# Performance work log

Measured on AMD Instinct MI355X. Metric: run time of the kernel, lower is better.

## Reference

```python
import jax, jax.numpy as jnp
import numpy as np

EPS = 1e-05
K = 32


def _knn_idx(xyz_B3N, k):
    # negative squared pairwise distance: -||xi||^2 + 2 xi.xj - ||xj||^2
    inner = 2.0 * jnp.einsum('bdn,bdm->bnm', xyz_B3N, xyz_B3N)  # [B,N,N]
    xx = jnp.sum(xyz_B3N ** 2, axis=1)  # [B,N]
    pd = inner - xx[:, :, None] - xx[:, None, :]
    _, idx = jax.lax.top_k(pd, k)  # [B,N,k] nearest (largest negative dist)
    return idx


def setup_inputs() -> dict:
    key = jax.random.key(0)
    k1, k2 = jax.random.split(key)
    B, N, C = 16, 4096, 64
    xyz_B3N = jax.random.normal(k1, (B, 3, N), dtype=jnp.float32)
    feats_BNC = jax.random.normal(k2, (B, N, C), dtype=jnp.float32)
    alpha = jnp.ones((C,), dtype=jnp.float32)
    beta = jnp.zeros((C,), dtype=jnp.float32)
    return {"xyz_B3N": xyz_B3N, "feats_BNC": feats_BNC, "alpha": alpha, "beta": beta}


def reference(xyz_B3N, feats_BNC, alpha, beta):
    idx = _knn_idx(xyz_B3N, K)  # [B,N,k]
    # gather neighbor features directly: [B,N,k,C]
    neigh = jax.vmap(lambda f, i: f[i])(feats_BNC, idx)
    offset = neigh - feats_BNC[:, :, None, :]  # [B,N,k,C]
    sigma = jnp.mean(offset ** 2)  # global scalar
    gaed = (offset / (sigma + EPS)) * alpha + beta
    pooled = jnp.max(gaed, axis=2)  # [B,N,C]
    return pooled
```

## Files before the change

kernel.cpp:

```cpp
#include <hip/hip_runtime.h>
#include <float.h>

#define BB 16
#define NN 4096
#define CC 64
#define KNN 32
#define NSLICE 16
#define SSZ 256
#define CKEEP 8
#define NQ 65536


__device__ __forceinline__ int lane_rank(unsigned long long m) {
    return __builtin_amdgcn_mbcnt_hi((unsigned)(m >> 32),
           __builtin_amdgcn_mbcnt_lo((unsigned)m, 0u));
}

__device__ __forceinline__ unsigned med3u(unsigned a, unsigned b, unsigned c) {
    unsigned d;
    asm("v_med3_u32 %0, %1, %2, %3" : "=v"(d) : "v"(a), "v"(b), "v"(c));
    return d;
}

#define UCHAIN8 \
  h07=med3u(ky,h07,h06); h06=med3u(ky,h06,h05); h05=med3u(ky,h05,h04); \
  h04=med3u(ky,h04,h03); h03=med3u(ky,h03,h02); h02=med3u(ky,h02,h01); \
  h01=med3u(ky,h01,h00); h00=(h00>ky)?h00:ky;

__global__ __launch_bounds__(256) void prep_kernel(
        const float* __restrict__ xyz, float4* __restrict__ pts4,
        int* __restrict__ flag_cnt) {
#pragma clang fp contract(off)
    const int p = blockIdx.x * 256 + threadIdx.x;
    if (p == 0) flag_cnt[0] = 0;
    const int b = p >> 12;
    const int i = p & (NN - 1);
    const float* xb = xyz + (size_t)b * (3 * NN);
    float x = xb[i], y = xb[NN + i], z = xb[2 * NN + i];
    float xx = ((x * x) + (y * y)) + (z * z);
    pts4[p] = make_float4(x, y, z, xx);
}

__global__ __launch_bounds__(256) void knn_select_kernel(
        const float4* __restrict__ pts4, unsigned* __restrict__ val_buf) {
#pragma clang fp contract(off)
    __shared__ float4 pts[SSZ];
    const int tid = threadIdx.x;
    const int blk = blockIdx.x;
    const int s = blk & 15;
    const int g = (blk >> 4) & 15;
    const int b = blk >> 8;
    const float4* pb = pts4 + (b << 12);

    pts[tid] = pb[(s << 8) | tid];
    const int q = (g << 8) | tid;
    const float4 qp = pb[q];
    const float qx = qp.x, qy = qp.y, qz = qp.z;
    const float nqxx = -qp.w;
    __syncthreads();

    unsigned h00=0,h01=0,h02=0,h03=0,h04=0,h05=0,h06=0,h07=0;
    const unsigned ibase = 4095u - (unsigned)(s << 8);
#pragma unroll 4
    for (int j = 0; j < SSZ; ++j) {
        float4 cp = pts[j];
        float dot = __builtin_fmaf(qz, cp.z, __builtin_fmaf(qy, cp.y, qx * cp.x));
        float pd = __builtin_fmaf(2.0f, dot, nqxx) - cp.w;
        pd = fminf(pd, 0.0f);
        unsigned ky = (~__float_as_uint(pd) & 0xFFFFF000u)
                      | (ibase - (unsigned)j);
        UCHAIN8
    }

    const int qg = (b << 12) | q;
    unsigned* vp = val_buf + (size_t)(s * CKEEP) * NQ + qg;
#define ST(t, ht) vp[(size_t)(t) * NQ] = ht;
    ST(0,h00) ST(1,h01) ST(2,h02) ST(3,h03)
    ST(4,h04) ST(5,h05) ST(6,h06) ST(7,h07)
#undef ST
}

__global__ __launch_bounds__(64) void knn_merge_kernel(
        const unsigned* __restrict__ val_buf, int* __restrict__ idx_out,
        int* __restrict__ flag_list, int* __restrict__ flag_cnt) {
    __shared__ unsigned lv[64 * 129];
    const int tid = threadIdx.x;
    const int qg = blockIdx.x * 64 + tid;
    unsigned* my = lv + tid * 129;
    for (int t = 0; t < 128; ++t) my[t] = val_buf[(size_t)t * NQ + qg];

    int p0=0,p1=0,p2=0,p3=0,p4=0,p5=0,p6=0,p7=0,
        p8=0,p9=0,p10=0,p11=0,p12=0,p13=0,p14=0,p15=0;
    unsigned v0 =my[0],  v1 =my[8],  v2 =my[16],  v3 =my[24];
    unsigned v4 =my[32], v5 =my[40], v6 =my[48],  v7 =my[56];
    unsigned v8 =my[64], v9 =my[72], v10=my[80],  v11=my[88];
    unsigned v12=my[96], v13=my[104],v14=my[112], v15=my[120];
    int* outp = idx_out + (size_t)qg * KNN;
    unsigned key32 = 0u, key33 = 0u;
    for (int step = 0; step < 33; ++step) {
        unsigned best = v0; int bp = 0;
        if (v1  > best) { best = v1;  bp = 1; }
        if (v2  > best) { best = v2;  bp = 2; }
        if (v3  > best) { best = v3;  bp = 3; }
        if (v4  > best) { best = v4;  bp = 4; }
        if (v5  > best) { best = v5;  bp = 5; }
        if (v6  > best) { best = v6;  bp = 6; }
        if (v7  > best) { best = v7;  bp = 7; }
        if (v8  > best) { best = v8;  bp = 8; }
        if (v9  > best) { best = v9;  bp = 9; }
        if (v10 > best) { best = v10; bp = 10; }
        if (v11 > best) { best = v11; bp = 11; }
        if (v12 > best) { best = v12; bp = 12; }
        if (v13 > best) { best = v13; bp = 13; }
        if (v14 > best) { best = v14; bp = 14; }
        if (v15 > best) { best = v15; bp = 15; }
        if (step == 32) { key33 = best; break; }
        outp[step] = 4095 - (int)(best & 4095u);
        if (step == 31) key32 = best;
        if      (bp==0)  { ++p0;  v0  = (p0 <8)?my[p0]      :0u; }
        else if (bp==1)  { ++p1;  v1  = (p1 <8)?my[8+p1]    :0u; }
        else if (bp==2)  { ++p2;  v2  = (p2 <8)?my[16+p2]   :0u; }
        else if (bp==3)  { ++p3;  v3  = (p3 <8)?my[24+p3]   :0u; }
        else if (bp==4)  { ++p4;  v4  = (p4 <8)?my[32+p4]   :0u; }
        else if (bp==5)  { ++p5;  v5  = (p5 <8)?my[40+p5]   :0u; }
        else if (bp==6)  { ++p6;  v6  = (p6 <8)?my[48+p6]   :0u; }
        else if (bp==7)  { ++p7;  v7  = (p7 <8)?my[56+p7]   :0u; }
        else if (bp==8)  { ++p8;  v8  = (p8 <8)?my[64+p8]   :0u; }
        else if (bp==9)  { ++p9;  v9  = (p9 <8)?my[72+p9]   :0u; }
        else if (bp==10) { ++p10; v10 = (p10<8)?my[80+p10]  :0u; }
        else if (bp==11) { ++p11; v11 = (p11<8)?my[88+p11]  :0u; }
        else if (bp==12) { ++p12; v12 = (p12<8)?my[96+p12]  :0u; }
        else if (bp==13) { ++p13; v13 = (p13<8)?my[104+p13] :0u; }
        else if (bp==14) { ++p14; v14 = (p14<8)?my[112+p14] :0u; }
        else             { ++p15; v15 = (p15<8)?my[120+p15] :0u; }
    }

    bool flag = ((key32 >> 12) == (key33 >> 12));
    for (int sl = 0; sl < 16; ++sl)
        flag = flag || (my[sl * 8 + 7] >= key33);
    if (flag) {
        int pos = atomicAdd(flag_cnt, 1);
        flag_list[pos] = qg;
    }
}

__global__ __launch_bounds__(256) void knn_fallback_kernel(
        const float* __restrict__ xyz, const int* __restrict__ flag_list,
        const int* __restrict__ flag_cnt, int* __restrict__ idx_out) {
#pragma clang fp contract(off)
    const int nflag = flag_cnt[0];
    const int lane = threadIdx.x & 63;
    const int wid = (blockIdx.x * 256 + threadIdx.x) >> 6;
    const int nw = (gridDim.x * 256) >> 6;
    for (int w = wid; w < nflag; w += nw) {
        const int qg = flag_list[w];
        const int b = qg >> 12;
        const int q = qg & (NN - 1);
        const float* xb = xyz + (size_t)b * (3 * NN);
        const float qx = xb[q], qy = xb[NN + q], qz = xb[2 * NN + q];
        const float qxx = ((qx * qx) + (qy * qy)) + (qz * qz);
        const float nqxx = -qxx;

        unsigned key[64];
#pragma unroll
        for (int i = 0; i < 64; ++i) {
            const int j = (i << 6) | lane;
            float x = xb[j], y = xb[NN + j], z = xb[2 * NN + j];
            float xxc = ((x * x) + (y * y)) + (z * z);
            float dot = __builtin_fmaf(qz, z, __builtin_fmaf(qy, y, qx * x));
            float pd = __builtin_fmaf(2.0f, dot, nqxx) - xxc;
            unsigned u = __float_as_uint(pd);
            key[i] = u ^ (unsigned)(((int)u >> 31) | 0x80000000);
        }

        unsigned cur = 0u;
        for (int bit = 31; bit >= 0; --bit) {
            const unsigned cand = cur | (1u << bit);
            int c = 0;
#pragma unroll
            for (int i = 0; i < 64; ++i) c += (key[i] >= cand) ? 1 : 0;
#pragma unroll
            for (int o = 32; o >= 1; o >>= 1) c += __shfl_xor(c, o, 64);
            if (c >= 32) cur = cand;
        }

        int ge = 0;
#pragma unroll
        for (int i = 0; i < 64; ++i) {
            ge += (key[i] > cur) ? 1 : 0;
            ge += (key[i] == cur) ? 0x10000 : 0;
        }
#pragma unroll
        for (int o = 32; o >= 1; o >>= 1) ge += __shfl_xor(ge, o, 64);
        const int gt_total = ge & 0xFFFF;
        const int budget = min(ge >> 16, 32 - gt_total);

        int* outp = idx_out + (size_t)qg * KNN;
        int slot = 0, neq = 0;
#pragma unroll
        for (int i = 0; i < 64; ++i) {
            const bool isgt = key[i] > cur;
            const bool iseq = key[i] == cur;
            const unsigned long long mgt = __ballot(isgt);
            const unsigned long long meq = __ballot(iseq);
            if (isgt) outp[slot + lane_rank(mgt)] = (i << 6) | lane;
            if (iseq) {
                const int r = neq + lane_rank(meq);
                if (r < budget) outp[gt_total + r] = (i << 6) | lane;
            }
            slot += __builtin_popcountll(mgt);
            neq += __builtin_popcountll(meq);
        }
    }
}

__global__ __launch_bounds__(256) void gather_minmax_kernel(
        const float* __restrict__ feats, const int* __restrict__ idx_in,
        float* __restrict__ mx_buf, float* __restrict__ mn_buf,
        double* __restrict__ partials) {
    const int tid = threadIdx.x;
    const int w = tid >> 6;
    const int lane = tid & 63;
    const int q = blockIdx.x * 4 + w;
    const int b = q >> 12;
    const float* fb = feats + (size_t)b * (NN * CC);
    const float center = feats[(size_t)q * CC + lane];
    const int* ip = idx_in + (size_t)q * KNN;

    float mx = -FLT_MAX, mn = FLT_MAX;
    double ss = 0.0;
#pragma unroll 4
    for (int k = 0; k < KNN; ++k) {
        int nb = ip[k];
        float v = fb[(size_t)nb * CC + lane];
        float off = v - center;
        mx = fmaxf(mx, off);
        mn = fminf(mn, off);
        double od = (double)off;
        ss = fma(od, od, ss);
    }
    mx_buf[(size_t)q * CC + lane] = mx;
    mn_buf[(size_t)q * CC + lane] = mn;

#pragma unroll
    for (int o = 32; o >= 1; o >>= 1) ss += __shfl_down(ss, o, 64);
    __shared__ double wsum[4];
    if (lane == 0) wsum[w] = ss;
    __syncthreads();
    if (tid == 0) partials[blockIdx.x] = (wsum[0] + wsum[1]) + (wsum[2] + wsum[3]);
}

__global__ __launch_bounds__(1024) void sigma_kernel(const double* __restrict__ partials,
                                                     float* __restrict__ sigma) {
    __shared__ double red[1024];
    double s = 0.0;
    for (int i = threadIdx.x; i < 16384; i += 1024) s += partials[i];
    red[threadIdx.x] = s;
    __syncthreads();
    for (int o = 512; o >= 1; o >>= 1) {
        if (threadIdx.x < o) red[threadIdx.x] += red[threadIdx.x + o];
        __syncthreads();
    }
    if (threadIdx.x == 0) sigma[0] = (float)(red[0] * (1.0 / 134217728.0));
}

__global__ __launch_bounds__(256) void finalize_kernel(
        const float* __restrict__ mx_buf, const float* __restrict__ mn_buf,
        const float* __restrict__ alpha, const float* __restrict__ beta,
        const float* __restrict__ sigma, float* __restrict__ out) {
#pragma clang fp contract(off)
    const int e = blockIdx.x * 256 + threadIdx.x;
    const int c = e & (CC - 1);
    const float s = sigma[0] + 1e-5f;
    const float a = alpha[c];
    const float bt = beta[c];
    const float off = (a >= 0.f) ? mx_buf[e] : mn_buf[e];
    const float t = off / s;
    out[e] = (t * a) + bt;
}

extern "C" void kernel_launch(void* const* d_in, const int* in_sizes, int n_in,
                              void* d_out, int out_size, void* d_ws, size_t ws_size,
                              hipStream_t stream) {
    (void)in_sizes; (void)n_in; (void)out_size; (void)ws_size;
    const float* xyz   = (const float*)d_in[0];
    const float* feats = (const float*)d_in[1];
    const float* alpha = (const float*)d_in[2];
    const float* beta  = (const float*)d_in[3];
    float* out = (float*)d_out;

    char* ws = (char*)d_ws;
    unsigned* val_buf  = (unsigned*)ws;
    float*    mx_buf   = (float*)ws;
    float*    mn_buf   = (float*)(ws + 16777216);
    int*      idx_buf  = (int*)(ws + 33554432);
    int*      flag_list= (int*)(ws + 41943040);
    int*      flag_cnt = (int*)(ws + 42205184);
    float4*   pts4     = (float4*)(ws + 42205248);
    double*   partials = (double*)(ws + 42205248);
    float*    sigma    = (float*)(ws + 43254784);

    prep_kernel<<<NQ / 256, 256, 0, stream>>>(xyz, pts4, flag_cnt);
    knn_select_kernel<<<BB * 16 * NSLICE, 256, 0, stream>>>(pts4, val_buf);
    knn_merge_kernel<<<NQ / 64, 64, 0, stream>>>(val_buf, idx_buf,
                                                 flag_list, flag_cnt);
    knn_fallback_kernel<<<256, 256, 0, stream>>>(xyz, flag_list, flag_cnt,
                                                 idx_buf);
    gather_minmax_kernel<<<NQ / 4, 256, 0, stream>>>(feats, idx_buf, mx_buf,
                                                     mn_buf, partials);
    sigma_kernel<<<1, 1024, 0, stream>>>(partials, sigma);
    finalize_kernel<<<(NQ * CC) / 256, 256, 0, stream>>>(mx_buf, mn_buf, alpha,
                                                         beta, sigma, out);
}
```

Measured before the change: 339.3 us.

## Fuse prep into KNN select, prefetch merge heads, vectorize gather to float2

```diff
diff --git a/kernel.cpp b/kernel.cpp
--- a/kernel.cpp
+++ b/kernel.cpp
@@ -27,36 +27,28 @@
   h04=med3u(ky,h04,h03); h03=med3u(ky,h03,h02); h02=med3u(ky,h02,h01); \
   h01=med3u(ky,h01,h00); h00=(h00>ky)?h00:ky;
 
-__global__ __launch_bounds__(256) void prep_kernel(
-        const float* __restrict__ xyz, float4* __restrict__ pts4,
+__global__ __launch_bounds__(256) void knn_select_kernel(
+        const float* __restrict__ xyz, unsigned* __restrict__ val_buf,
         int* __restrict__ flag_cnt) {
-#pragma clang fp contract(off)
-    const int p = blockIdx.x * 256 + threadIdx.x;
-    if (p == 0) flag_cnt[0] = 0;
-    const int b = p >> 12;
-    const int i = p & (NN - 1);
-    const float* xb = xyz + (size_t)b * (3 * NN);
-    float x = xb[i], y = xb[NN + i], z = xb[2 * NN + i];
-    float xx = ((x * x) + (y * y)) + (z * z);
-    pts4[p] = make_float4(x, y, z, xx);
-}
-
-__global__ __launch_bounds__(256) void knn_select_kernel(
-        const float4* __restrict__ pts4, unsigned* __restrict__ val_buf) {
 #pragma clang fp contract(off)
     __shared__ float4 pts[SSZ];
     const int tid = threadIdx.x;
     const int blk = blockIdx.x;
+    if (blk == 0 && tid == 0) flag_cnt[0] = 0;
     const int s = blk & 15;
     const int g = (blk >> 4) & 15;
     const int b = blk >> 8;
-    const float4* pb = pts4 + (b << 12);
-
-    pts[tid] = pb[(s << 8) | tid];
+    const float* xb = xyz + (size_t)b * (3 * NN);
+
+    {
+        const int i = (s << 8) | tid;
+        float x = xb[i], y = xb[NN + i], z = xb[2 * NN + i];
+        float xx = ((x * x) + (y * y)) + (z * z);
+        pts[tid] = make_float4(x, y, z, xx);
+    }
     const int q = (g << 8) | tid;
-    const float4 qp = pb[q];
-    const float qx = qp.x, qy = qp.y, qz = qp.z;
-    const float nqxx = -qp.w;
+    const float qx = xb[q], qy = xb[NN + q], qz = xb[2 * NN + q];
+    const float nqxx = -(((qx * qx) + (qy * qy)) + (qz * qz));
     __syncthreads();
 
     unsigned h00=0,h01=0,h02=0,h03=0,h04=0,h05=0,h06=0,h07=0;
@@ -91,10 +83,14 @@
 
     int p0=0,p1=0,p2=0,p3=0,p4=0,p5=0,p6=0,p7=0,
         p8=0,p9=0,p10=0,p11=0,p12=0,p13=0,p14=0,p15=0;
-    unsigned v0 =my[0],  v1 =my[8],  v2 =my[16],  v3 =my[24];
-    unsigned v4 =my[32], v5 =my[40], v6 =my[48],  v7 =my[56];
-    unsigned v8 =my[64], v9 =my[72], v10=my[80],  v11=my[88];
-    unsigned v12=my[96], v13=my[104],v14=my[112], v15=my[120];
+    unsigned v0 =my[0],  w0 =my[1];   unsigned v1 =my[8],  w1 =my[9];
+    unsigned v2 =my[16], w2 =my[17];  unsigned v3 =my[24], w3 =my[25];
+    unsigned v4 =my[32], w4 =my[33];  unsigned v5 =my[40], w5 =my[41];
+    unsigned v6 =my[48], w6 =my[49];  unsigned v7 =my[56], w7 =my[57];
+    unsigned v8 =my[64], w8 =my[65];  unsigned v9 =my[72], w9 =my[73];
+    unsigned v10=my[80], w10=my[81];  unsigned v11=my[88], w11=my[89];
+    unsigned v12=my[96], w12=my[97];  unsigned v13=my[104],w13=my[105];
+    unsigned v14=my[112],w14=my[113]; unsigned v15=my[120],w15=my[121];
     int* outp = idx_out + (size_t)qg * KNN;
     unsigned key32 = 0u, key33 = 0u;
     for (int step = 0; step < 33; ++step) {
@@ -117,22 +113,22 @@
         if (step == 32) { key33 = best; break; }
         outp[step] = 4095 - (int)(best & 4095u);
         if (step == 31) key32 = best;
-        if      (bp==0)  { ++p0;  v0  = (p0 <8)?my[p0]      :0u; }
-        else if (bp==1)  { ++p1;  v1  = (p1 <8)?my[8+p1]    :0u; }
-        else if (bp==2)  { ++p2;  v2  = (p2 <8)?my[16+p2]   :0u; }
-        else if (bp==3)  { ++p3;  v3  = (p3 <8)?my[24+p3]   :0u; }
-        else if (bp==4)  { ++p4;  v4  = (p4 <8)?my[32+p4]   :0u; }
-        else if (bp==5)  { ++p5;  v5  = (p5 <8)?my[40+p5]   :0u; }
-        else if (bp==6)  { ++p6;  v6  = (p6 <8)?my[48+p6]   :0u; }
-        else if (bp==7)  { ++p7;  v7  = (p7 <8)?my[56+p7]   :0u; }
-        else if (bp==8)  { ++p8;  v8  = (p8 <8)?my[64+p8]   :0u; }
-        else if (bp==9)  { ++p9;  v9  = (p9 <8)?my[72+p9]   :0u; }
-        else if (bp==10) { ++p10; v10 = (p10<8)?my[80+p10]  :0u; }
-        else if (bp==11) { ++p11; v11 = (p11<8)?my[88+p11]  :0u; }
-        else if (bp==12) { ++p12; v12 = (p12<8)?my[96+p12]  :0u; }
-        else if (bp==13) { ++p13; v13 = (p13<8)?my[104+p13] :0u; }
-        else if (bp==14) { ++p14; v14 = (p14<8)?my[112+p14] :0u; }
-        else             { ++p15; v15 = (p15<8)?my[120+p15] :0u; }
+        if      (bp==0)  { v0 =w0;  ++p0;  w0  = (p0 <7)?my[p0 +1]    :0u; }
+        else if (bp==1)  { v1 =w1;  ++p1;  w1  = (p1 <7)?my[8+p1 +1]  :0u; }
+        else if (bp==2)  { v2 =w2;  ++p2;  w2  = (p2 <7)?my[16+p2+1]  :0u; }
+        else if (bp==3)  { v3 =w3;  ++p3;  w3  = (p3 <7)?my[24+p3+1]  :0u; }
+        else if (bp==4)  { v4 =w4;  ++p4;  w4  = (p4 <7)?my[32+p4+1]  :0u; }
+        else if (bp==5)  { v5 =w5;  ++p5;  w5  = (p5 <7)?my[40+p5+1]  :0u; }
+        else if (bp==6)  { v6 =w6;  ++p6;  w6  = (p6 <7)?my[48+p6+1]  :0u; }
+        else if (bp==7)  { v7 =w7;  ++p7;  w7  = (p7 <7)?my[56+p7+1]  :0u; }
+        else if (bp==8)  { v8 =w8;  ++p8;  w8  = (p8 <7)?my[64+p8+1]  :0u; }
+        else if (bp==9)  { v9 =w9;  ++p9;  w9  = (p9 <7)?my[72+p9+1]  :0u; }
+        else if (bp==10) { v10=w10; ++p10; w10 = (p10<7)?my[80+p10+1] :0u; }
+        else if (bp==11) { v11=w11; ++p11; w11 = (p11<7)?my[88+p11+1] :0u; }
+        else if (bp==12) { v12=w12; ++p12; w12 = (p12<7)?my[96+p12+1] :0u; }
+        else if (bp==13) { v13=w13; ++p13; w13 = (p13<7)?my[104+p13+1]:0u; }
+        else if (bp==14) { v14=w14; ++p14; w14 = (p14<7)?my[112+p14+1]:0u; }
+        else             { v15=w15; ++p15; w15 = (p15<7)?my[120+p15+1]:0u; }
     }
 
     bool flag = ((key32 >> 12) == (key33 >> 12));
@@ -219,42 +215,49 @@
         float* __restrict__ mx_buf, float* __restrict__ mn_buf,
         double* __restrict__ partials) {
     const int tid = threadIdx.x;
-    const int w = tid >> 6;
-    const int lane = tid & 63;
-    const int q = blockIdx.x * 4 + w;
+    const int qw = tid >> 5;
+    const int lane32 = tid & 31;
+    const int q = blockIdx.x * 8 + qw;
     const int b = q >> 12;
-    const float* fb = feats + (size_t)b * (NN * CC);
-    const float center = feats[(size_t)q * CC + lane];
+    const float2* fb2 = (const float2*)(feats + (size_t)b * (NN * CC));
+    const int ql = q & (NN - 1);
+    const float2 c2 = fb2[(size_t)ql * 32 + lane32];
     const int* ip = idx_in + (size_t)q * KNN;
 
-    float mx = -FLT_MAX, mn = FLT_MAX;
+    float mx0 = -FLT_MAX, mn0 = FLT_MAX, mx1 = -FLT_MAX, mn1 = FLT_MAX;
     double ss = 0.0;
 #pragma unroll 4
     for (int k = 0; k < KNN; ++k) {
         int nb = ip[k];
-        float v = fb[(size_t)nb * CC + lane];
-        float off = v - center;
-        mx = fmaxf(mx, off);
-        mn = fminf(mn, off);
-        double od = (double)off;
-        ss = fma(od, od, ss);
-    }
-    mx_buf[(size_t)q * CC + lane] = mx;
-    mn_buf[(size_t)q * CC + lane] = mn;
-
-#pragma unroll
-    for (int o = 32; o >= 1; o >>= 1) ss += __shfl_down(ss, o, 64);
-    __shared__ double wsum[4];
-    if (lane == 0) wsum[w] = ss;
+        float2 v = fb2[(size_t)nb * 32 + lane32];
+        float o0 = v.x - c2.x;
+        float o1 = v.y - c2.y;
+        mx0 = fmaxf(mx0, o0); mn0 = fminf(mn0, o0);
+        mx1 = fmaxf(mx1, o1); mn1 = fminf(mn1, o1);
+        double d0 = (double)o0, d1 = (double)o1;
+        ss = fma(d0, d0, ss);
+        ss = fma(d1, d1, ss);
+    }
+    ((float2*)mx_buf)[(size_t)q * 32 + lane32] = make_float2(mx0, mx1);
+    ((float2*)mn_buf)[(size_t)q * 32 + lane32] = make_float2(mn0, mn1);
+
+#pragma unroll
+    for (int o = 16; o >= 1; o >>= 1) ss += __shfl_down(ss, o, 64);
+    __shared__ double wsum[8];
+    if (lane32 == 0) wsum[qw] = ss;
     __syncthreads();
-    if (tid == 0) partials[blockIdx.x] = (wsum[0] + wsum[1]) + (wsum[2] + wsum[3]);
+    if (tid == 0) {
+        double t = ((wsum[0] + wsum[1]) + (wsum[2] + wsum[3]))
+                 + ((wsum[4] + wsum[5]) + (wsum[6] + wsum[7]));
+        partials[blockIdx.x] = t;
+    }
 }
 
 __global__ __launch_bounds__(1024) void sigma_kernel(const double* __restrict__ partials,
                                                      float* __restrict__ sigma) {
     __shared__ double red[1024];
     double s = 0.0;
-    for (int i = threadIdx.x; i < 16384; i += 1024) s += partials[i];
+    for (int i = threadIdx.x; i < 8192; i += 1024) s += partials[i];
     red[threadIdx.x] = s;
     __syncthreads();
     for (int o = 512; o >= 1; o >>= 1) {
@@ -296,17 +299,16 @@
     int*      idx_buf  = (int*)(ws + 33554432);
     int*      flag_list= (int*)(ws + 41943040);
     int*      flag_cnt = (int*)(ws + 42205184);
-    float4*   pts4     = (float4*)(ws + 42205248);
     double*   partials = (double*)(ws + 42205248);
     float*    sigma    = (float*)(ws + 43254784);
 
-    prep_kernel<<<NQ / 256, 256, 0, stream>>>(xyz, pts4, flag_cnt);
-    knn_select_kernel<<<BB * 16 * NSLICE, 256, 0, stream>>>(pts4, val_buf);
+    knn_select_kernel<<<BB * 16 * NSLICE, 256, 0, stream>>>(xyz, val_buf,
+                                                            flag_cnt);
     knn_merge_kernel<<<NQ / 64, 64, 0, stream>>>(val_buf, idx_buf,
                                                  flag_list, flag_cnt);
     knn_fallback_kernel<<<256, 256, 0, stream>>>(xyz, flag_list, flag_cnt,
                                                  idx_buf);
-    gather_minmax_kernel<<<NQ / 4, 256, 0, stream>>>(feats, idx_buf, mx_buf,
+    gather_minmax_kernel<<<NQ / 8, 256, 0, stream>>>(feats, idx_buf, mx_buf,
                                                      mn_buf, partials);
     sigma_kernel<<<1, 1024, 0, stream>>>(partials, sigma);
     finalize_kernel<<<(NQ * CC) / 256, 256, 0, stream>>>(mx_buf, mn_buf, alpha,
```

Result: no change. 336.0 us (-1.0%).
